# Kernel optimization log

Hardware: AMD Instinct MI355X
Metric: run time of the kernel (lower is better)

Reference implementation:

```python
import jax, jax.numpy as jnp
import numpy as np


def euler_xyz_to_matrix(angles):
    # pytorch3d euler_angles_to_matrix(angles, 'XYZ') = R_X(a0) @ R_Y(a1) @ R_Z(a2)
    ax, ay, az = angles[..., 0], angles[..., 1], angles[..., 2]
    cx, sx = jnp.cos(ax), jnp.sin(ax)
    cy, sy = jnp.cos(ay), jnp.sin(ay)
    cz, sz = jnp.cos(az), jnp.sin(az)
    one = jnp.ones_like(ax)
    zero = jnp.zeros_like(ax)
    Rx = jnp.stack([one, zero, zero, zero, cx, -sx, zero, sx, cx], axis=-1).reshape(*ax.shape, 3, 3)
    Ry = jnp.stack([cy, zero, sy, zero, one, zero, -sy, zero, cy], axis=-1).reshape(*ax.shape, 3, 3)
    Rz = jnp.stack([cz, -sz, zero, sz, cz, zero, zero, zero, one], axis=-1).reshape(*ax.shape, 3, 3)
    return Rx @ Ry @ Rz


def chamfer_bidir(x, y):
    # x, y: [R, I, N, 3]. Squared-distance chamfer, mean point reduction, per (R,I) batch.
    x2 = jnp.sum(x * x, axis=-1)  # [R,I,N]
    y2 = jnp.sum(y * y, axis=-1)  # [R,I,N]
    # d2[r,i,n,m] = |x_n - y_m|^2
    d2 = x2[..., :, None] + y2[..., None, :] - 2.0 * jnp.einsum('rind,rimd->rinm', x, y)
    cham_x = jnp.mean(jnp.min(d2, axis=-1), axis=-1)  # x -> nearest y
    cham_y = jnp.mean(jnp.min(d2, axis=-2), axis=-1)  # y -> nearest x
    return cham_x + cham_y  # [R, I]


def setup_inputs() -> dict:
    key = jax.random.key(0)
    k1, k2, k3, k4 = jax.random.split(key, 4)
    R, I, N = 4, 16, 2048
    source_points = jax.random.normal(k1, (R, I, N, 3), dtype=jnp.float32)
    target_points = jax.random.normal(k2, (I, N, 3), dtype=jnp.float32)
    rotation = 0.1 * jax.random.normal(k3, (R, I, 3), dtype=jnp.float32)
    translation = 0.1 * jax.random.normal(k4, (R, I, 3), dtype=jnp.float32)
    scale = jnp.ones((R, I), dtype=jnp.float32)
    return {
        'source_points': source_points,
        'target_points': target_points,
        'rotation': rotation,
        'translation': translation,
        'scale': scale,
    }


def reference(source_points, target_points, rotation, translation, scale):
    R, I, N, _ = source_points.shape
    rot = euler_xyz_to_matrix(rotation)  # [R,I,3,3]
    # Transform per original: 4x4 matrix with rows [:3,:] scaled by `scale`,
    # so p' = scale * (rot @ p + translation).
    transformed = scale[..., None, None] * (
        jnp.einsum('rind,rikd->rink', source_points, rot) + translation[..., None, :]
    )  # [R,I,N,3]
    # target_points [I,N,3] broadcast to [R,I,N,3] (original repeats along R)
    target = jnp.broadcast_to(target_points[None], transformed.shape)
    # original calls chamfer_distance(target, transformed): x=target, y=transformed
    return chamfer_bidir(target, transformed)  # [R, I]
```

## Files before the change

### kernel.cpp

```cpp
#include <hip/hip_runtime.h>
#include <math.h>

#define RDIM 4
#define IDIM 16
#define NPAIR (RDIM * IDIM)
#define NPTS 2048
#define THREADS 256
#define ROWSB 64
#define RBLOCKS (NPTS / ROWSB)

typedef __attribute__((ext_vector_type(8))) short bf16x8;
typedef __attribute__((ext_vector_type(4))) float f32x4;

__device__ __forceinline__ unsigned int f2bf(float f) {
    union { float f; unsigned int u; } v; v.f = f;
    return (v.u + 0x7FFFu + ((v.u >> 16) & 1u)) >> 16;
}
__device__ __forceinline__ float bf2f(unsigned int h) {
    union { unsigned int u; float f; } v; v.u = h << 16; return v.f;
}

__device__ __forceinline__ void make_rot(const float* __restrict__ rotv, int pair,
                                         float& r00, float& r01, float& r02,
                                         float& r10, float& r11, float& r12,
                                         float& r20, float& r21, float& r22) {
    const float ax = rotv[pair * 3 + 0];
    const float ay = rotv[pair * 3 + 1];
    const float az = rotv[pair * 3 + 2];
    float sx, cx, sy, cy, sz, cz;
    sincosf(ax, &sx, &cx);
    sincosf(ay, &sy, &cy);
    sincosf(az, &sz, &cz);
    r00 = cy * cz;                r01 = -cy * sz;               r02 = sy;
    r10 = cx * sz + sx * sy * cz; r11 = cx * cz - sx * sy * sz; r12 = -sx * cy;
    r20 = sx * sz - cx * sy * cz; r21 = sx * cz + cx * sy * sz; r22 = cx * cy;
}

__device__ __forceinline__ uint4 make_rec(float v0, float v1, float v2, float n2) {
    const unsigned int h0 = f2bf(-2.0f * v0);
    const unsigned int h1 = f2bf(-2.0f * v1);
    const unsigned int h2 = f2bf(-2.0f * v2);
    const unsigned int l0 = f2bf(-2.0f * v0 - bf2f(h0));
    const unsigned int l1 = f2bf(-2.0f * v1 - bf2f(h1));
    const unsigned int l2 = f2bf(-2.0f * v2 - bf2f(h2));
    const unsigned int n2h = f2bf(n2);
    const unsigned int n2l = f2bf(n2 - bf2f(n2h));
    return make_uint4(h0 | (h1 << 16), h2 | (l0 << 16), l1 | (l2 << 16), n2h | (n2l << 16));
}

__global__ __launch_bounds__(THREADS)
void prep(const float* __restrict__ src, const float* __restrict__ tgt,
          const float* __restrict__ rotv, const float* __restrict__ trav,
          const float* __restrict__ scal,
          uint4* __restrict__ Yb, uint4* __restrict__ Xb,
          float* __restrict__ y2f, float* __restrict__ x2f)
{
    const int b = blockIdx.x;
    const int tid = threadIdx.x;
    if (b < NPAIR) {
        const int pair = b;
        float r00, r01, r02, r10, r11, r12, r20, r21, r22;
        make_rot(rotv, pair, r00, r01, r02, r10, r11, r12, r20, r21, r22);
        const float t0 = trav[pair * 3 + 0];
        const float t1 = trav[pair * 3 + 1];
        const float t2 = trav[pair * 3 + 2];
        const float s  = scal[pair];
        const float* __restrict__ srcp = src + (size_t)pair * NPTS * 3;
#pragma unroll
        for (int u = 0; u < NPTS / THREADS; ++u) {
            const int m = u * THREADS + tid;
            const float p0 = srcp[m * 3 + 0];
            const float p1 = srcp[m * 3 + 1];
            const float p2 = srcp[m * 3 + 2];
            const float y0 = s * fmaf(r00, p0, fmaf(r01, p1, fmaf(r02, p2, t0)));
            const float y1 = s * fmaf(r10, p0, fmaf(r11, p1, fmaf(r12, p2, t1)));
            const float y2 = s * fmaf(r20, p0, fmaf(r21, p1, fmaf(r22, p2, t2)));
            const float n2 = y0 * y0 + y1 * y1 + y2 * y2;
            y2f[(size_t)pair * NPTS + m] = n2;
            Yb[(size_t)pair * NPTS + m] = make_rec(y0, y1, y2, n2);
        }
    } else {
        const int i = b - NPAIR;
        const float* __restrict__ tgtp = tgt + (size_t)i * NPTS * 3;
#pragma unroll
        for (int u = 0; u < NPTS / THREADS; ++u) {
            const int m = u * THREADS + tid;
            const float x0 = tgtp[m * 3 + 0];
            const float x1 = tgtp[m * 3 + 1];
            const float x2 = tgtp[m * 3 + 2];
            const float n2 = x0 * x0 + x1 * x1 + x2 * x2;
            x2f[(size_t)i * NPTS + m] = n2;
            Xb[(size_t)i * NPTS + m] = make_rec(x0, x1, x2, n2);
        }
    }
}

__global__ __launch_bounds__(THREADS, 4)
void chamfer_main(const float* __restrict__ src, const float* __restrict__ tgt,
                  const float* __restrict__ rotv, const float* __restrict__ trav,
                  const float* __restrict__ scal,
                  const uint4* __restrict__ Yb, const uint4* __restrict__ Xb,
                  const float* __restrict__ y2f, const float* __restrict__ x2f,
                  float* __restrict__ out)
{
    __shared__ uint4 sB[NPTS];
    __shared__ alignas(16) unsigned short rowk[ROWSB * 32];
    __shared__ float rowq2[ROWSB];
    __shared__ float rowpart[4][ROWSB];

    const int pair  = blockIdx.x;
    const int rb    = blockIdx.y;
    const int passB = blockIdx.z;
    const int i     = pair & (IDIM - 1);
    const int tid   = threadIdx.x;
    const int lane  = tid & 63;
    const int w     = tid >> 6;
    const int g     = lane >> 4;
    const int c15   = lane & 15;

    const uint4* __restrict__ gB = (passB == 0) ? (Yb + (size_t)pair * NPTS)
                                                : (Xb + (size_t)i * NPTS);
#pragma unroll
    for (int j = 0; j < NPTS / THREADS; ++j)
        sB[j * THREADS + tid] = gB[j * THREADS + tid];

    if (tid < ROWSB) {
        const int n = rb * ROWSB + tid;
        float q0, q1, q2v;
        if (passB == 0) {
            const float* __restrict__ tgtp = tgt + (size_t)i * NPTS * 3;
            q0 = tgtp[n * 3 + 0]; q1 = tgtp[n * 3 + 1]; q2v = tgtp[n * 3 + 2];
            rowq2[tid] = x2f[(size_t)i * NPTS + n];
        } else {
            float r00, r01, r02, r10, r11, r12, r20, r21, r22;
            make_rot(rotv, pair, r00, r01, r02, r10, r11, r12, r20, r21, r22);
            const float t0 = trav[pair * 3 + 0];
            const float t1 = trav[pair * 3 + 1];
            const float t2 = trav[pair * 3 + 2];
            const float s  = scal[pair];
            const float* __restrict__ srcp = src + (size_t)pair * NPTS * 3;
            const float p0 = srcp[n * 3 + 0];
            const float p1 = srcp[n * 3 + 1];
            const float p2 = srcp[n * 3 + 2];
            q0  = s * fmaf(r00, p0, fmaf(r01, p1, fmaf(r02, p2, t0)));
            q1  = s * fmaf(r10, p0, fmaf(r11, p1, fmaf(r12, p2, t1)));
            q2v = s * fmaf(r20, p0, fmaf(r21, p1, fmaf(r22, p2, t2)));
            rowq2[tid] = y2f[(size_t)pair * NPTS + n];
        }
        const unsigned int h0 = f2bf(q0), h1 = f2bf(q1), h2 = f2bf(q2v);
        const unsigned int l0 = f2bf(q0 - bf2f(h0));
        const unsigned int l1 = f2bf(q1 - bf2f(h1));
        const unsigned int l2 = f2bf(q2v - bf2f(h2));
        const unsigned int one = 0x3F80u;
        uint4* rk = (uint4*)&rowk[tid * 32];
        rk[0] = make_uint4(h0 | (h1 << 16), h2 | (l0 << 16), l1 | (l2 << 16), one | (one << 16));
        rk[1] = make_uint4(l0 | (l1 << 16), l2 | (h0 << 16), h1 | (h2 << 16), 0u);
        rk[2] = make_uint4(0u, 0u, 0u, 0u);
        rk[3] = make_uint4(0u, 0u, 0u, 0u);
    }
    __syncthreads();

    bf16x8 afrag[4];
#pragma unroll
    for (int rt = 0; rt < 4; ++rt)
        afrag[rt] = *(const bf16x8*)&rowk[(rt * 16 + c15) * 32 + (g << 3)];

    float rowmin[4][4];
#pragma unroll
    for (int rt = 0; rt < 4; ++rt)
#pragma unroll
        for (int r = 0; r < 4; ++r) rowmin[rt][r] = 3.4e38f;

    const f32x4 zero4 = {0.0f, 0.0f, 0.0f, 0.0f};
    const int cw = w << 9;

#pragma unroll 4
    for (int t = 0; t < 32; ++t) {
        const bf16x8 bfrag = *(const bf16x8*)&sB[cw + (t << 4) + c15];
#pragma unroll
        for (int rt = 0; rt < 4; ++rt) {
            f32x4 d = __builtin_amdgcn_mfma_f32_16x16x32_bf16(afrag[rt], bfrag, zero4, 0, 0, 0);
            rowmin[rt][0] = fminf(rowmin[rt][0], d[0]);
            rowmin[rt][1] = fminf(rowmin[rt][1], d[1]);
            rowmin[rt][2] = fminf(rowmin[rt][2], d[2]);
            rowmin[rt][3] = fminf(rowmin[rt][3], d[3]);
        }
    }

#pragma unroll
    for (int rt = 0; rt < 4; ++rt)
#pragma unroll
        for (int r = 0; r < 4; ++r) {
            float v = rowmin[rt][r];
            v = fminf(v, __shfl_xor(v, 1, 64));
            v = fminf(v, __shfl_xor(v, 2, 64));
            v = fminf(v, __shfl_xor(v, 4, 64));
            v = fminf(v, __shfl_xor(v, 8, 64));
            if (c15 == 0) rowpart[w][rt * 16 + (g << 2) + r] = v;
        }
    __syncthreads();
    if (tid < ROWSB) {
        const float m = fminf(fminf(rowpart[0][tid], rowpart[1][tid]),
                              fminf(rowpart[2][tid], rowpart[3][tid]));
        float v = m + rowq2[tid];
#pragma unroll
        for (int off = 32; off > 0; off >>= 1)
            v += __shfl_down(v, off, 64);
        if (tid == 0) atomicAdd(&out[pair], v * (1.0f / NPTS));
    }
}

extern "C" void kernel_launch(void* const* d_in, const int* in_sizes, int n_in,
                              void* d_out, int out_size, void* d_ws, size_t ws_size,
                              hipStream_t stream) {
    const float* src  = (const float*)d_in[0];
    const float* tgt  = (const float*)d_in[1];
    const float* rotv = (const float*)d_in[2];
    const float* trav = (const float*)d_in[3];
    const float* scal = (const float*)d_in[4];
    float* out = (float*)d_out;

    char* ws = (char*)d_ws;
    uint4* Yb  = (uint4*)ws;
    uint4* Xb  = (uint4*)(ws + (size_t)NPAIR * NPTS * 16);
    float* y2f = (float*)(ws + (size_t)(NPAIR + IDIM) * NPTS * 16);
    float* x2f = y2f + (size_t)NPAIR * NPTS;

    hipMemsetAsync(out, 0, NPAIR * sizeof(float), stream);

    prep<<<NPAIR + IDIM, THREADS, 0, stream>>>(src, tgt, rotv, trav, scal, Yb, Xb, y2f, x2f);

    dim3 grid(NPAIR, RBLOCKS, 2);
    chamfer_main<<<grid, THREADS, 0, stream>>>(src, tgt, rotv, trav, scal,
                                               Yb, Xb, y2f, x2f, out);
}
```

Before: 103.2 us.

## Switch to 32x32x16 MFMA with 256-row blocks and precomputed A fragments

Replaces the 16x16x32 MFMA tiling with 32x32x16 bf16 MFMA. Each block now handles 256 query rows, so each wave owns 64 rows and sweeps all 2048 columns instead of a quarter of them. The A operands are now precomputed in the prep kernel and loaded from global memory, rather than being rebuilt per block from raw points with a rotation. The row-min reduction moves to an LDS scratch transpose, and the squared norm is recomputed from the bf16 hi/lo parts. The aim is to do less wasted K padding and setup per block, and to cut the grid from 4096 to 1024 blocks. The cost is more register pressure (32 accumulators per wave), less parallelism, and extra workspace traffic.

New measurement: 84.86 us. 17.7% less time.

```diff
diff --git a/kernel.cpp b/kernel.cpp
--- a/kernel.cpp
+++ b/kernel.cpp
@@ -3,13 +3,17 @@
 
 #define RDIM 4
 #define IDIM 16
-#define NPAIR (RDIM * IDIM)
+#define NPAIR 64
 #define NPTS 2048
 #define THREADS 256
-#define ROWSB 64
-#define RBLOCKS (NPTS / ROWSB)
+#define ROWSB 256
+#define RBLK (NPTS / ROWSB)
+#define TILES (NPTS / 32)
+#define SCRS 68
+#define ONEBF 0x3F80u
 
 typedef __attribute__((ext_vector_type(8))) short bf16x8;
+typedef __attribute__((ext_vector_type(16))) float f32x16;
 typedef __attribute__((ext_vector_type(4))) float f32x4;
 
 __device__ __forceinline__ unsigned int f2bf(float f) {
@@ -36,24 +40,31 @@
     r20 = sx * sz - cx * sy * cz; r21 = sx * cz + cx * sy * sz; r22 = cx * cy;
 }
 
-__device__ __forceinline__ uint4 make_rec(float v0, float v1, float v2, float n2) {
-    const unsigned int h0 = f2bf(-2.0f * v0);
-    const unsigned int h1 = f2bf(-2.0f * v1);
-    const unsigned int h2 = f2bf(-2.0f * v2);
-    const unsigned int l0 = f2bf(-2.0f * v0 - bf2f(h0));
-    const unsigned int l1 = f2bf(-2.0f * v1 - bf2f(h1));
-    const unsigned int l2 = f2bf(-2.0f * v2 - bf2f(h2));
-    const unsigned int n2h = f2bf(n2);
-    const unsigned int n2l = f2bf(n2 - bf2f(n2h));
-    return make_uint4(h0 | (h1 << 16), h2 | (l0 << 16), l1 | (l2 << 16), n2h | (n2l << 16));
+__device__ __forceinline__ uint4 brec(float v0, float v1, float v2) {
+    const float b0 = -2.0f * v0, b1 = -2.0f * v1, b2 = -2.0f * v2;
+    const unsigned int h0 = f2bf(b0), h1 = f2bf(b1), h2 = f2bf(b2);
+    const unsigned int l0 = f2bf(b0 - bf2f(h0));
+    const unsigned int l1 = f2bf(b1 - bf2f(h1));
+    const unsigned int l2 = f2bf(b2 - bf2f(h2));
+    const float n2 = v0 * v0 + v1 * v1 + v2 * v2;
+    const unsigned int nh = f2bf(n2), nl = f2bf(n2 - bf2f(nh));
+    return make_uint4(h0 | (h1 << 16), h2 | (l0 << 16), l1 | (l2 << 16), nh | (nl << 16));
+}
+__device__ __forceinline__ void arec(float q0, float q1, float q2, uint4& a0, uint4& a1) {
+    const unsigned int h0 = f2bf(q0), h1 = f2bf(q1), h2 = f2bf(q2);
+    const unsigned int l0 = f2bf(q0 - bf2f(h0));
+    const unsigned int l1 = f2bf(q1 - bf2f(h1));
+    const unsigned int l2 = f2bf(q2 - bf2f(h2));
+    a0 = make_uint4(h0 | (h1 << 16), h2 | (l0 << 16), l1 | (l2 << 16), ONEBF);
+    a1 = make_uint4(l0 | (l1 << 16), l2 | (h0 << 16), h1 | (h2 << 16), ONEBF << 16);
 }
 
 __global__ __launch_bounds__(THREADS)
 void prep(const float* __restrict__ src, const float* __restrict__ tgt,
           const float* __restrict__ rotv, const float* __restrict__ trav,
           const float* __restrict__ scal,
-          uint4* __restrict__ Yb, uint4* __restrict__ Xb,
-          float* __restrict__ y2f, float* __restrict__ x2f)
+          uint4* __restrict__ Yb, uint4* __restrict__ Ya,
+          uint4* __restrict__ Xb, uint4* __restrict__ Xa)
 {
     const int b = blockIdx.x;
     const int tid = threadIdx.x;
@@ -75,9 +86,11 @@
             const float y0 = s * fmaf(r00, p0, fmaf(r01, p1, fmaf(r02, p2, t0)));
             const float y1 = s * fmaf(r10, p0, fmaf(r11, p1, fmaf(r12, p2, t1)));
             const float y2 = s * fmaf(r20, p0, fmaf(r21, p1, fmaf(r22, p2, t2)));
-            const float n2 = y0 * y0 + y1 * y1 + y2 * y2;
-            y2f[(size_t)pair * NPTS + m] = n2;
-            Yb[(size_t)pair * NPTS + m] = make_rec(y0, y1, y2, n2);
+            Yb[(size_t)pair * NPTS + m] = brec(y0, y1, y2);
+            uint4 a0, a1;
+            arec(y0, y1, y2, a0, a1);
+            Ya[((size_t)pair * NPTS + m) * 2 + 0] = a0;
+            Ya[((size_t)pair * NPTS + m) * 2 + 1] = a1;
         }
     } else {
         const int i = b - NPAIR;
@@ -88,25 +101,25 @@
             const float x0 = tgtp[m * 3 + 0];
             const float x1 = tgtp[m * 3 + 1];
             const float x2 = tgtp[m * 3 + 2];
-            const float n2 = x0 * x0 + x1 * x1 + x2 * x2;
-            x2f[(size_t)i * NPTS + m] = n2;
-            Xb[(size_t)i * NPTS + m] = make_rec(x0, x1, x2, n2);
+            Xb[(size_t)i * NPTS + m] = brec(x0, x1, x2);
+            uint4 a0, a1;
+            arec(x0, x1, x2, a0, a1);
+            Xa[((size_t)i * NPTS + m) * 2 + 0] = a0;
+            Xa[((size_t)i * NPTS + m) * 2 + 1] = a1;
         }
     }
 }
 
-__global__ __launch_bounds__(THREADS, 4)
-void chamfer_main(const float* __restrict__ src, const float* __restrict__ tgt,
-                  const float* __restrict__ rotv, const float* __restrict__ trav,
-                  const float* __restrict__ scal,
-                  const uint4* __restrict__ Yb, const uint4* __restrict__ Xb,
-                  const float* __restrict__ y2f, const float* __restrict__ x2f,
+__global__ __launch_bounds__(THREADS, 3)
+void chamfer_main(const uint4* __restrict__ Yb, const uint4* __restrict__ Ya,
+                  const uint4* __restrict__ Xb, const uint4* __restrict__ Xa,
                   float* __restrict__ out)
 {
-    __shared__ uint4 sB[NPTS];
-    __shared__ alignas(16) unsigned short rowk[ROWSB * 32];
-    __shared__ float rowq2[ROWSB];
-    __shared__ float rowpart[4][ROWSB];
+    __shared__ alignas(16) unsigned char smem[34816 + 8192];
+    __shared__ float wsum[4];
+    unsigned short* sB = (unsigned short*)smem;
+    float* scratch = (float*)smem;
+    unsigned short* sA = (unsigned short*)(smem + 34816);
 
     const int pair  = blockIdx.x;
     const int rb    = blockIdx.y;
@@ -115,98 +128,80 @@
     const int tid   = threadIdx.x;
     const int lane  = tid & 63;
     const int w     = tid >> 6;
-    const int g     = lane >> 4;
-    const int c15   = lane & 15;
+    const int c31   = lane & 31;
+    const int h     = lane >> 5;
 
     const uint4* __restrict__ gB = (passB == 0) ? (Yb + (size_t)pair * NPTS)
                                                 : (Xb + (size_t)i * NPTS);
-#pragma unroll
-    for (int j = 0; j < NPTS / THREADS; ++j)
-        sB[j * THREADS + tid] = gB[j * THREADS + tid];
-
-    if (tid < ROWSB) {
-        const int n = rb * ROWSB + tid;
-        float q0, q1, q2v;
-        if (passB == 0) {
-            const float* __restrict__ tgtp = tgt + (size_t)i * NPTS * 3;
-            q0 = tgtp[n * 3 + 0]; q1 = tgtp[n * 3 + 1]; q2v = tgtp[n * 3 + 2];
-            rowq2[tid] = x2f[(size_t)i * NPTS + n];
-        } else {
-            float r00, r01, r02, r10, r11, r12, r20, r21, r22;
-            make_rot(rotv, pair, r00, r01, r02, r10, r11, r12, r20, r21, r22);
-            const float t0 = trav[pair * 3 + 0];
-            const float t1 = trav[pair * 3 + 1];
-            const float t2 = trav[pair * 3 + 2];
-            const float s  = scal[pair];
-            const float* __restrict__ srcp = src + (size_t)pair * NPTS * 3;
-            const float p0 = srcp[n * 3 + 0];
-            const float p1 = srcp[n * 3 + 1];
-            const float p2 = srcp[n * 3 + 2];
-            q0  = s * fmaf(r00, p0, fmaf(r01, p1, fmaf(r02, p2, t0)));
-            q1  = s * fmaf(r10, p0, fmaf(r11, p1, fmaf(r12, p2, t1)));
-            q2v = s * fmaf(r20, p0, fmaf(r21, p1, fmaf(r22, p2, t2)));
-            rowq2[tid] = y2f[(size_t)pair * NPTS + n];
-        }
-        const unsigned int h0 = f2bf(q0), h1 = f2bf(q1), h2 = f2bf(q2v);
-        const unsigned int l0 = f2bf(q0 - bf2f(h0));
-        const unsigned int l1 = f2bf(q1 - bf2f(h1));
-        const unsigned int l2 = f2bf(q2v - bf2f(h2));
-        const unsigned int one = 0x3F80u;
-        uint4* rk = (uint4*)&rowk[tid * 32];
-        rk[0] = make_uint4(h0 | (h1 << 16), h2 | (l0 << 16), l1 | (l2 << 16), one | (one << 16));
-        rk[1] = make_uint4(l0 | (l1 << 16), l2 | (h0 << 16), h1 | (h2 << 16), 0u);
-        rk[2] = make_uint4(0u, 0u, 0u, 0u);
-        rk[3] = make_uint4(0u, 0u, 0u, 0u);
+    const uint4* __restrict__ gA = (passB == 0)
+        ? (Xa + ((size_t)i * NPTS + rb * ROWSB) * 2)
+        : (Ya + ((size_t)pair * NPTS + rb * ROWSB) * 2);
+
+#pragma unroll
+    for (int j = 0; j < 8; ++j)
+        ((uint4*)sB)[j * THREADS + tid] = gB[j * THREADS + tid];
+    ((uint4*)sA)[tid] = gA[tid];
+    ((uint4*)sA)[THREADS + tid] = gA[THREADS + tid];
+    __syncthreads();
+
+    bf16x8 af[2];
+    af[0] = *(const bf16x8*)&sA[(w * 64 + c31) * 16 + h * 8];
+    af[1] = *(const bf16x8*)&sA[(w * 64 + 32 + c31) * 16 + h * 8];
+
+    float mn[2][16];
+#pragma unroll
+    for (int rt = 0; rt < 2; ++rt)
+#pragma unroll
+        for (int j = 0; j < 16; ++j) mn[rt][j] = 3.4e38f;
+
+    const f32x16 zero16 = {0,0,0,0, 0,0,0,0, 0,0,0,0, 0,0,0,0};
+
+#pragma unroll 4
+    for (int t = 0; t < TILES; ++t) {
+        const bf16x8 bf = *(const bf16x8*)&sB[(t * 32 + c31) * 8];
+        const f32x16 d0 = __builtin_amdgcn_mfma_f32_32x32x16_bf16(af[0], bf, zero16, 0, 0, 0);
+        const f32x16 d1 = __builtin_amdgcn_mfma_f32_32x32x16_bf16(af[1], bf, zero16, 0, 0, 0);
+#pragma unroll
+        for (int j = 0; j < 16; ++j) {
+            mn[0][j] = fminf(mn[0][j], d0[j]);
+            mn[1][j] = fminf(mn[1][j], d1[j]);
+        }
     }
     __syncthreads();
 
-    bf16x8 afrag[4];
-#pragma unroll
-    for (int rt = 0; rt < 4; ++rt)
-        afrag[rt] = *(const bf16x8*)&rowk[(rt * 16 + c15) * 32 + (g << 3)];
-
-    float rowmin[4][4];
-#pragma unroll
-    for (int rt = 0; rt < 4; ++rt)
-#pragma unroll
-        for (int r = 0; r < 4; ++r) rowmin[rt][r] = 3.4e38f;
-
-    const f32x4 zero4 = {0.0f, 0.0f, 0.0f, 0.0f};
-    const int cw = w << 9;
-
-#pragma unroll 4
-    for (int t = 0; t < 32; ++t) {
-        const bf16x8 bfrag = *(const bf16x8*)&sB[cw + (t << 4) + c15];
-#pragma unroll
-        for (int rt = 0; rt < 4; ++rt) {
-            f32x4 d = __builtin_amdgcn_mfma_f32_16x16x32_bf16(afrag[rt], bfrag, zero4, 0, 0, 0);
-            rowmin[rt][0] = fminf(rowmin[rt][0], d[0]);
-            rowmin[rt][1] = fminf(rowmin[rt][1], d[1]);
-            rowmin[rt][2] = fminf(rowmin[rt][2], d[2]);
-            rowmin[rt][3] = fminf(rowmin[rt][3], d[3]);
-        }
-    }
-
-#pragma unroll
-    for (int rt = 0; rt < 4; ++rt)
-#pragma unroll
-        for (int r = 0; r < 4; ++r) {
-            float v = rowmin[rt][r];
-            v = fminf(v, __shfl_xor(v, 1, 64));
-            v = fminf(v, __shfl_xor(v, 2, 64));
-            v = fminf(v, __shfl_xor(v, 4, 64));
-            v = fminf(v, __shfl_xor(v, 8, 64));
-            if (c15 == 0) rowpart[w][rt * 16 + (g << 2) + r] = v;
-        }
-    __syncthreads();
-    if (tid < ROWSB) {
-        const float m = fminf(fminf(rowpart[0][tid], rowpart[1][tid]),
-                              fminf(rowpart[2][tid], rowpart[3][tid]));
-        float v = m + rowq2[tid];
-#pragma unroll
-        for (int off = 32; off > 0; off >>= 1)
-            v += __shfl_down(v, off, 64);
-        if (tid == 0) atomicAdd(&out[pair], v * (1.0f / NPTS));
+#pragma unroll
+    for (int rt = 0; rt < 2; ++rt)
+#pragma unroll
+        for (int g2 = 0; g2 < 4; ++g2) {
+            const int rowb = rt * 32 + 8 * g2 + 4 * h;
+            f32x4 v4;
+            v4[0] = mn[rt][g2 * 4 + 0];
+            v4[1] = mn[rt][g2 * 4 + 1];
+            v4[2] = mn[rt][g2 * 4 + 2];
+            v4[3] = mn[rt][g2 * 4 + 3];
+            *(f32x4*)&scratch[(w * 32 + c31) * SCRS + rowb] = v4;
+        }
+    __syncthreads();
+
+    float m = scratch[(w * 32) * SCRS + lane];
+#pragma unroll
+    for (int c = 1; c < 32; ++c)
+        m = fminf(m, scratch[(w * 32 + c) * SCRS + lane]);
+
+    const unsigned short* ar = &sA[tid * 16];
+    const float q0 = bf2f(ar[0]) + bf2f(ar[3]);
+    const float q1 = bf2f(ar[1]) + bf2f(ar[4]);
+    const float q2 = bf2f(ar[2]) + bf2f(ar[5]);
+    float v = m + q0 * q0 + q1 * q1 + q2 * q2;
+
+#pragma unroll
+    for (int off = 32; off > 0; off >>= 1)
+        v += __shfl_down(v, off, 64);
+    if (lane == 0) wsum[w] = v;
+    __syncthreads();
+    if (tid == 0) {
+        const float tot = wsum[0] + wsum[1] + wsum[2] + wsum[3];
+        atomicAdd(&out[pair], tot * (1.0f / NPTS));
     }
 }
 
@@ -221,16 +216,15 @@
     float* out = (float*)d_out;
 
     char* ws = (char*)d_ws;
-    uint4* Yb  = (uint4*)ws;
-    uint4* Xb  = (uint4*)(ws + (size_t)NPAIR * NPTS * 16);
-    float* y2f = (float*)(ws + (size_t)(NPAIR + IDIM) * NPTS * 16);
-    float* x2f = y2f + (size_t)NPAIR * NPTS;
+    uint4* Yb = (uint4*)ws;
+    uint4* Ya = (uint4*)(ws + (size_t)NPAIR * NPTS * 16);
+    uint4* Xb = (uint4*)(ws + (size_t)NPAIR * NPTS * 48);
+    uint4* Xa = (uint4*)(ws + (size_t)NPAIR * NPTS * 48 + (size_t)IDIM * NPTS * 16);
 
     hipMemsetAsync(out, 0, NPAIR * sizeof(float), stream);
 
-    prep<<<NPAIR + IDIM, THREADS, 0, stream>>>(src, tgt, rotv, trav, scal, Yb, Xb, y2f, x2f);
-
-    dim3 grid(NPAIR, RBLOCKS, 2);
-    chamfer_main<<<grid, THREADS, 0, stream>>>(src, tgt, rotv, trav, scal,
-                                               Yb, Xb, y2f, x2f, out);
-}
+    prep<<<NPAIR + IDIM, THREADS, 0, stream>>>(src, tgt, rotv, trav, scal, Yb, Ya, Xb, Xa);
+
+    dim3 grid(NPAIR, RBLK, 2);
+    chamfer_main<<<grid, THREADS, 0, stream>>>(Yb, Ya, Xb, Xa, out);
+}
```
